# Kernel tuning notes

Hardware: AMD Instinct MI355X
Metric: run time of the kernel (lower is better)

The kernel has to match this reference:

```python
import jax, jax.numpy as jnp
import numpy as np

N_NODES = 100000
N_EDGES = 1600000
IN_CH, HID_CH, LAT = 32, 32, 16


def _gcn_layer(h, W, b, src, dst, norm):
    # PyG GCNConv: h' = scatter_add(norm * (h W)[src] -> dst) + b
    h = h @ W                                   # [N, out]
    msg = h[src] * norm[:, None]                # [E+N, out] gather
    out = jax.ops.segment_sum(msg, dst, num_segments=N_NODES)
    return out + b


def setup_inputs() -> dict:
    key = jax.random.key(0)
    ks = jax.random.split(key, 8)
    x = jax.random.normal(ks[0], (N_NODES, IN_CH), dtype=jnp.float32)
    edge_index = jax.random.randint(ks[1], (2, N_EDGES), 0, N_NODES, dtype=jnp.int32)
    def glorot(k, fan_in, fan_out):
        lim = np.sqrt(6.0 / (fan_in + fan_out)).astype(np.float32)
        return jax.random.uniform(k, (fan_in, fan_out), jnp.float32, -lim, lim)
    return {
        "x": x,
        "edge_index": edge_index,
        "W1": glorot(ks[2], IN_CH, HID_CH),
        "b1": jnp.zeros((HID_CH,), jnp.float32),
        "Wmu": glorot(ks[3], HID_CH, LAT),
        "bmu": jnp.zeros((LAT,), jnp.float32),
        "Wlv": glorot(ks[4], HID_CH, LAT),
        "blv": jnp.zeros((LAT,), jnp.float32),
    }


def reference(x, edge_index, W1, b1, Wmu, bmu, Wlv, blv):
    # Add self-loops (GCNConv default add_self_loops=True)
    loops = jnp.arange(N_NODES, dtype=edge_index.dtype)
    src = jnp.concatenate([edge_index[0], loops])
    dst = jnp.concatenate([edge_index[1], loops])
    # Symmetric normalization: deg over destinations, norm = d^-1/2[src] * d^-1/2[dst]
    deg = jax.ops.segment_sum(jnp.ones_like(dst, dtype=x.dtype), dst,
                              num_segments=N_NODES)
    dinv = jnp.where(deg > 0, jax.lax.rsqrt(deg), 0.0)
    norm = dinv[src] * dinv[dst]                # [E+N]

    h = jax.nn.relu(_gcn_layer(x, W1, b1, src, dst, norm))
    mu = _gcn_layer(h, Wmu, bmu, src, dst, norm)
    logvar = _gcn_layer(h, Wlv, blv, src, dst, norm)
    return (mu, logvar)
```

## Files before the change

kernel.cpp:

```cpp
#include <hip/hip_runtime.h>
#include <hip/hip_fp16.h>

#define N_NODES 100000
#define N_EDGES 1600000
#define NCB 391
#define CAPC 4736
#define P1_CHUNK 4096
#define P1_BLOCKS 391
#define BKN 256
#define NBF_G 1563


__global__ __launch_bounds__(512) void k_part1(const int* __restrict__ src,
                                               const int* __restrict__ dst,
                                               int* __restrict__ cursor1,
                                               unsigned* __restrict__ packed1) {
    __shared__ int bh[NCB];
    __shared__ int base[NCB];
    int t = threadIdx.x;
    if (t < NCB) bh[t] = 0;
    __syncthreads();
    int e0 = blockIdx.x * P1_CHUNK;
    int e1 = e0 + P1_CHUNK; if (e1 > N_EDGES) e1 = N_EDGES;
    int d[8], s[8];
#pragma unroll
    for (int j = 0; j < 8; ++j) {
        int e = e0 + t + j * 512;
        if (e < e1) { d[j] = dst[e]; s[j] = src[e]; } else d[j] = -1;
    }
#pragma unroll
    for (int j = 0; j < 8; ++j)
        if (d[j] >= 0) atomicAdd(&bh[((unsigned)d[j]) >> 8], 1);
    __syncthreads();
    if (t < NCB) {
        int c = bh[t];
        base[t] = t * CAPC + ((c > 0) ? atomicAdd(&cursor1[t], c) : 0);
        bh[t] = 0;
    }
    __syncthreads();
#pragma unroll
    for (int j = 0; j < 8; ++j) {
        if (d[j] < 0) continue;
        unsigned dd = (unsigned)d[j];
        int b = dd >> 8;
        int r = atomicAdd(&bh[b], 1);
        int pos = base[b] + r;
        if (pos < (b + 1) * CAPC)
            packed1[pos] = ((dd & 255u) << 17) | (unsigned)s[j];
    }
}

__global__ __launch_bounds__(512) void k_csrx(const unsigned* __restrict__ packed1,
                                              const int* __restrict__ cursor1,
                                              const float* __restrict__ x,
                                              const float* __restrict__ W1,
                                              int* __restrict__ rowBeg,
                                              int* __restrict__ rowEnd,
                                              float* __restrict__ dinv,
                                              int* __restrict__ srcSorted,
                                              __half* __restrict__ p1) {
    __shared__ int cnt[BKN];
    __shared__ int scn[BKN];
    __shared__ int cur[BKN];
    __shared__ float sW[1024];
    int t = threadIdx.x;
    int b = blockIdx.x;
    int seg0 = b * CAPC;
    int cc = cursor1[b]; if (cc > CAPC) cc = CAPC;
    int segEnd = seg0 + cc;
    if (t < BKN) cnt[t] = 0;
    for (int i = t; i < 1024; i += 512) sW[i] = W1[i];
    __syncthreads();
    for (int i = seg0 + t; i < segEnd; i += 512)
        atomicAdd(&cnt[packed1[i] >> 17], 1);
    __syncthreads();
    int v = (t < BKN) ? cnt[t] : 0;
    if (t < BKN) scn[t] = v;
    __syncthreads();
    for (int off = 1; off < BKN; off <<= 1) {
        int u = (t < BKN && t >= off) ? scn[t - off] : 0;
        __syncthreads();
        if (t < BKN) scn[t] += u;
        __syncthreads();
    }
    int node = b * BKN + t;
    if (t < BKN) {
        int start = seg0 + scn[t] - v;
        if (node < N_NODES) {
            rowBeg[node] = start;
            rowEnd[node] = start + v;
            dinv[node] = rsqrtf((float)(v + 1));
        }
        cur[t] = start;
    }
    __syncthreads();
    for (int i = seg0 + t; i < segEnd; i += 512) {
        unsigned pk = packed1[i];
        int pos = atomicAdd(&cur[pk >> 17], 1);
        srcSorted[pos] = (int)(pk & 0x1FFFFu);
    }
    int lane = t & 31;
    for (int r = (t >> 5); r < BKN; r += 16) {
        int nd = b * BKN + r;
        if (nd > N_NODES) break;
        if (nd == N_NODES) {
            p1[nd * 32 + lane] = __float2half(0.f);
            continue;
        }
        float xv = x[nd * 32 + lane];
        float a = 0.f;
#pragma unroll
        for (int k = 0; k < 32; ++k) {
            float xk = __shfl(xv, k, 32);
            a += xk * sW[k * 32 + lane];
        }
        float di = rsqrtf((float)(cnt[r] + 1));
        p1[nd * 32 + lane] = __float2half(di * a);
    }
}

__device__ __forceinline__ __half2 h2of(const float4& v, int c) {
    return reinterpret_cast<const __half2*>(&v)[c];
}

__device__ __forceinline__ void gatherRow4(const int* __restrict__ srcSorted,
                                           const float4* __restrict__ P,
                                           int beg, int end, int l,
                                           float* __restrict__ acc ) {
    for (int base = beg; base < end; base += 8) {
        int i0 = base + l, i1 = base + 4 + l;
        int sA = (i0 < end) ? srcSorted[i0] : N_NODES;
        int sB = (i1 < end) ? srcSorted[i1] : N_NODES;
        float4 v0 = P[__shfl(sA, 0, 4) * 4 + l];
        float4 v1 = P[__shfl(sA, 1, 4) * 4 + l];
        float4 v2 = P[__shfl(sA, 2, 4) * 4 + l];
        float4 v3 = P[__shfl(sA, 3, 4) * 4 + l];
        float4 v4 = P[__shfl(sB, 0, 4) * 4 + l];
        float4 v5 = P[__shfl(sB, 1, 4) * 4 + l];
        float4 v6 = P[__shfl(sB, 2, 4) * 4 + l];
        float4 v7 = P[__shfl(sB, 3, 4) * 4 + l];
#pragma unroll
        for (int c = 0; c < 4; ++c) {
            __half2 s01 = __hadd2(h2of(v0, c), h2of(v1, c));
            __half2 s23 = __hadd2(h2of(v2, c), h2of(v3, c));
            __half2 s45 = __hadd2(h2of(v4, c), h2of(v5, c));
            __half2 s67 = __hadd2(h2of(v6, c), h2of(v7, c));
            __half2 sum = __hadd2(__hadd2(s01, s23), __hadd2(s45, s67));
            float2 f = __half22float2(sum);
            acc[2 * c]     += f.x;
            acc[2 * c + 1] += f.y;
        }
    }
}

__global__ __launch_bounds__(256) void k_gx2(const int* __restrict__ rowBeg,
                                             const int* __restrict__ rowEnd,
                                             const int* __restrict__ srcSorted,
                                             const __half* __restrict__ p1,
                                             const float* __restrict__ dinv,
                                             const float* __restrict__ b1,
                                             const float* __restrict__ Wmu,
                                             const float* __restrict__ Wlv,
                                             __half* __restrict__ p2) {
    __shared__ float sW[1024];
    __shared__ float sB[32];
    int t = threadIdx.x;
    for (int i = t; i < 1024; i += 256) {
        int k = i >> 5, oc = i & 31;
        sW[i] = (oc < 16) ? Wmu[k * 16 + oc] : Wlv[k * 16 + (oc - 16)];
    }
    if (t < 32) sB[t] = b1[t];
    __syncthreads();
    int l = t & 3;
    int node = blockIdx.x * 64 + (t >> 2);
    if (node > N_NODES) return;
    const float4* P = (const float4*)p1;
    if (node == N_NODES) {
        ((float4*)p2)[node * 4 + l] = make_float4(0.f, 0.f, 0.f, 0.f);
        return;
    }
    float acc[8] = {0.f, 0.f, 0.f, 0.f, 0.f, 0.f, 0.f, 0.f};
    gatherRow4(srcSorted, P, rowBeg[node], rowEnd[node], l, acc);
    float di = dinv[node];
    float4 ps = P[node * 4 + l];
    float h[8];
#pragma unroll
    for (int c = 0; c < 4; ++c) {
        float2 f = __half22float2(h2of(ps, c));
        h[2 * c]     = fmaxf(di * (acc[2 * c]     + f.x) + sB[8 * l + 2 * c],     0.f);
        h[2 * c + 1] = fmaxf(di * (acc[2 * c + 1] + f.y) + sB[8 * l + 2 * c + 1], 0.f);
    }
    float o[8] = {0.f, 0.f, 0.f, 0.f, 0.f, 0.f, 0.f, 0.f};
    const float4* W4 = (const float4*)sW;
#pragma unroll
    for (int m = 0; m < 4; ++m) {
#pragma unroll
        for (int j = 0; j < 8; ++j) {
            float hk = __shfl(h[j], m, 4);
            int k = 8 * m + j;
            float4 wa = W4[k * 8 + 2 * l];
            float4 wb = W4[k * 8 + 2 * l + 1];
            o[0] += hk * wa.x; o[1] += hk * wa.y; o[2] += hk * wa.z; o[3] += hk * wa.w;
            o[4] += hk * wb.x; o[5] += hk * wb.y; o[6] += hk * wb.z; o[7] += hk * wb.w;
        }
    }
    __half2 r0 = __floats2half2_rn(di * o[0], di * o[1]);
    __half2 r1 = __floats2half2_rn(di * o[2], di * o[3]);
    __half2 r2 = __floats2half2_rn(di * o[4], di * o[5]);
    __half2 r3 = __floats2half2_rn(di * o[6], di * o[7]);
    float4 st;
    st.x = *reinterpret_cast<float*>(&r0);
    st.y = *reinterpret_cast<float*>(&r1);
    st.z = *reinterpret_cast<float*>(&r2);
    st.w = *reinterpret_cast<float*>(&r3);
    ((float4*)p2)[node * 4 + l] = st;
}

__global__ __launch_bounds__(256) void k_gfin(const int* __restrict__ rowBeg,
                                              const int* __restrict__ rowEnd,
                                              const int* __restrict__ srcSorted,
                                              const __half* __restrict__ p2,
                                              const float* __restrict__ dinv,
                                              const float* __restrict__ bmu,
                                              const float* __restrict__ blv,
                                              float* __restrict__ out) {
    __shared__ float sB[32];
    int t = threadIdx.x;
    if (t < 32) sB[t] = (t < 16) ? bmu[t] : blv[t - 16];
    __syncthreads();
    int l = t & 3;
    int node = blockIdx.x * 64 + (t >> 2);
    if (node >= N_NODES) return;
    const float4* P = (const float4*)p2;
    float acc[8] = {0.f, 0.f, 0.f, 0.f, 0.f, 0.f, 0.f, 0.f};
    gatherRow4(srcSorted, P, rowBeg[node], rowEnd[node], l, acc);
    float di = dinv[node];
    float4 ps = P[node * 4 + l];
    float v[8];
#pragma unroll
    for (int c = 0; c < 4; ++c) {
        float2 f = __half22float2(h2of(ps, c));
        v[2 * c]     = di * (acc[2 * c]     + f.x) + sB[8 * l + 2 * c];
        v[2 * c + 1] = di * (acc[2 * c + 1] + f.y) + sB[8 * l + 2 * c + 1];
    }
    float4 o0 = make_float4(v[0], v[1], v[2], v[3]);
    float4 o1 = make_float4(v[4], v[5], v[6], v[7]);
    float4* dst4 = (l < 2) ? (float4*)out
                           : (float4*)(out + (size_t)N_NODES * 16);
    int b4 = node * 4 + (l & 1) * 2;
    dst4[b4]     = o0;
    dst4[b4 + 1] = o1;
}

extern "C" void kernel_launch(void* const* d_in, const int* in_sizes, int n_in,
                              void* d_out, int out_size, void* d_ws, size_t ws_size,
                              hipStream_t stream) {
    const float* x   = (const float*)d_in[0];
    const int*   ei  = (const int*)d_in[1];
    const float* W1  = (const float*)d_in[2];
    const float* b1  = (const float*)d_in[3];
    const float* Wmu = (const float*)d_in[4];
    const float* bmu = (const float*)d_in[5];
    const float* Wlv = (const float*)d_in[6];
    const float* blv = (const float*)d_in[7];
    float* out = (float*)d_out;

    const int* src = ei;
    const int* dst = ei + N_EDGES;

    size_t off = 0;
    int* cursor1 = (int*)d_ws;                          off += NCB;
    int* rowBeg  = (int*)d_ws + off;                    off += N_NODES;
    int* rowEnd  = (int*)d_ws + off;                    off += N_NODES;
    float* dinv  = (float*)((int*)d_ws + off);          off += N_NODES;
    off = (off + 63) & ~(size_t)63;
    unsigned* packed1 = (unsigned*)((int*)d_ws + off);  off += (size_t)NCB * CAPC;
    off = (off + 63) & ~(size_t)63;
    int* srcSorted    = (int*)d_ws + off;               off += (size_t)NCB * CAPC;
    off = (off + 63) & ~(size_t)63;
    __half* p1h = (__half*)((int*)d_ws + off);          off += (size_t)(N_NODES + 1) * 16;
    off = (off + 63) & ~(size_t)63;
    __half* p2h = (__half*)((int*)d_ws + off);

    hipMemsetAsync(d_ws, 0, (size_t)NCB * sizeof(int), stream);
    k_part1<<<P1_BLOCKS, 512, 0, stream>>>(src, dst, cursor1, packed1);
    k_csrx <<<NCB, 512, 0, stream>>>(packed1, cursor1, x, W1,
                                     rowBeg, rowEnd, dinv, srcSorted, p1h);
    k_gx2  <<<NBF_G, 256, 0, stream>>>(rowBeg, rowEnd, srcSorted, p1h, dinv,
                                       b1, Wmu, Wlv, p2h);
    k_gfin <<<NBF_G, 256, 0, stream>>>(rowBeg, rowEnd, srcSorted, p2h, dinv,
                                       bmu, blv, out);
}
```

Baseline: 188.0 us.

## Halve CSR bucket width and reuse first-pass atomic ranks for scatter

Buckets now cover 128 destination nodes instead of 256, which doubles the bucket count and shrinks per-bucket capacity. k_part1 runs 1024 threads per block and keeps the rank returned by the counting atomic, so the second scatter pass needs no atomics. k_csrx likewise holds up to 5 packed entries per thread in registers and reuses their counting ranks, dropping the second global read and the cursor atomics. The cost is twice as many csrx blocks, each with the full W1 load and the scan, plus tighter capacity limits (2560 per bucket, 5 elements per thread) that could overflow for skewed degree distributions.

```diff
diff --git a/kernel.cpp b/kernel.cpp
--- a/kernel.cpp
+++ b/kernel.cpp
@@ -3,50 +3,49 @@
 
 #define N_NODES 100000
 #define N_EDGES 1600000
-#define NCB 391
-#define CAPC 4736
+#define NCB 782
+#define CAPC 2560
 #define P1_CHUNK 4096
 #define P1_BLOCKS 391
-#define BKN 256
+#define BKN 128
+#define EPT 5
 #define NBF_G 1563
 
 
-__global__ __launch_bounds__(512) void k_part1(const int* __restrict__ src,
-                                               const int* __restrict__ dst,
-                                               int* __restrict__ cursor1,
-                                               unsigned* __restrict__ packed1) {
+__global__ __launch_bounds__(1024) void k_part1(const int* __restrict__ src,
+                                                const int* __restrict__ dst,
+                                                int* __restrict__ cursor1,
+                                                unsigned* __restrict__ packed1) {
     __shared__ int bh[NCB];
     __shared__ int base[NCB];
     int t = threadIdx.x;
-    if (t < NCB) bh[t] = 0;
+    for (int i = t; i < NCB; i += 1024) bh[i] = 0;
     __syncthreads();
     int e0 = blockIdx.x * P1_CHUNK;
     int e1 = e0 + P1_CHUNK; if (e1 > N_EDGES) e1 = N_EDGES;
-    int d[8], s[8];
-#pragma unroll
-    for (int j = 0; j < 8; ++j) {
-        int e = e0 + t + j * 512;
+    int d[4], s[4], r[4];
+#pragma unroll
+    for (int j = 0; j < 4; ++j) {
+        int e = e0 + t + j * 1024;
         if (e < e1) { d[j] = dst[e]; s[j] = src[e]; } else d[j] = -1;
     }
 #pragma unroll
-    for (int j = 0; j < 8; ++j)
-        if (d[j] >= 0) atomicAdd(&bh[((unsigned)d[j]) >> 8], 1);
-    __syncthreads();
-    if (t < NCB) {
-        int c = bh[t];
-        base[t] = t * CAPC + ((c > 0) ? atomicAdd(&cursor1[t], c) : 0);
-        bh[t] = 0;
-    }
-    __syncthreads();
-#pragma unroll
-    for (int j = 0; j < 8; ++j) {
+    for (int j = 0; j < 4; ++j)
+        if (d[j] >= 0) r[j] = atomicAdd(&bh[((unsigned)d[j]) >> 7], 1);
+    __syncthreads();
+    for (int i = t; i < NCB; i += 1024) {
+        int c = bh[i];
+        base[i] = i * CAPC + ((c > 0) ? atomicAdd(&cursor1[i], c) : 0);
+    }
+    __syncthreads();
+#pragma unroll
+    for (int j = 0; j < 4; ++j) {
         if (d[j] < 0) continue;
         unsigned dd = (unsigned)d[j];
-        int b = dd >> 8;
-        int r = atomicAdd(&bh[b], 1);
-        int pos = base[b] + r;
+        int b = dd >> 7;
+        int pos = base[b] + r[j];
         if (pos < (b + 1) * CAPC)
-            packed1[pos] = ((dd & 255u) << 17) | (unsigned)s[j];
+            packed1[pos] = ((dd & 127u) << 17) | (unsigned)s[j];
     }
 }
 
@@ -61,7 +60,7 @@
                                               __half* __restrict__ p1) {
     __shared__ int cnt[BKN];
     __shared__ int scn[BKN];
-    __shared__ int cur[BKN];
+    __shared__ int stt[BKN];
     __shared__ float sW[1024];
     int t = threadIdx.x;
     int b = blockIdx.x;
@@ -71,8 +70,15 @@
     if (t < BKN) cnt[t] = 0;
     for (int i = t; i < 1024; i += 512) sW[i] = W1[i];
     __syncthreads();
-    for (int i = seg0 + t; i < segEnd; i += 512)
-        atomicAdd(&cnt[packed1[i] >> 17], 1);
+    unsigned pk[EPT]; int rk[EPT];
+#pragma unroll
+    for (int j = 0; j < EPT; ++j) {
+        int i = seg0 + t + j * 512;
+        pk[j] = (i < segEnd) ? packed1[i] : 0xFFFFFFFFu;
+    }
+#pragma unroll
+    for (int j = 0; j < EPT; ++j)
+        if (pk[j] != 0xFFFFFFFFu) rk[j] = atomicAdd(&cnt[pk[j] >> 17], 1);
     __syncthreads();
     int v = (t < BKN) ? cnt[t] : 0;
     if (t < BKN) scn[t] = v;
@@ -86,18 +92,19 @@
     int node = b * BKN + t;
     if (t < BKN) {
         int start = seg0 + scn[t] - v;
+        stt[t] = start;
         if (node < N_NODES) {
             rowBeg[node] = start;
             rowEnd[node] = start + v;
             dinv[node] = rsqrtf((float)(v + 1));
         }
-        cur[t] = start;
-    }
-    __syncthreads();
-    for (int i = seg0 + t; i < segEnd; i += 512) {
-        unsigned pk = packed1[i];
-        int pos = atomicAdd(&cur[pk >> 17], 1);
-        srcSorted[pos] = (int)(pk & 0x1FFFFu);
+    }
+    __syncthreads();
+#pragma unroll
+    for (int j = 0; j < EPT; ++j) {
+        if (pk[j] == 0xFFFFFFFFu) continue;
+        int pos = stt[pk[j] >> 17] + rk[j];
+        srcSorted[pos] = (int)(pk[j] & 0x1FFFFu);
     }
     int lane = t & 31;
     for (int r = (t >> 5); r < BKN; r += 16) {
@@ -283,7 +290,7 @@
     __half* p2h = (__half*)((int*)d_ws + off);
 
     hipMemsetAsync(d_ws, 0, (size_t)NCB * sizeof(int), stream);
-    k_part1<<<P1_BLOCKS, 512, 0, stream>>>(src, dst, cursor1, packed1);
+    k_part1<<<P1_BLOCKS, 1024, 0, stream>>>(src, dst, cursor1, packed1);
     k_csrx <<<NCB, 512, 0, stream>>>(packed1, cursor1, x, W1,
                                      rowBeg, rowEnd, dinv, srcSorted, p1h);
     k_gx2  <<<NBF_G, 256, 0, stream>>>(rowBeg, rowEnd, srcSorted, p1h, dinv,
```

New measurement: 184.7 us. No clear change (-1.8%).
